# Optimization experiments

Measured on AMD Instinct MI355X. Metric: run time of the kernel, lower is better.

## Reference

```python
import jax, jax.numpy as jnp
import numpy as np

N_TREES = 10
N_DEPTH = 8
IN_DIM = 2048
CLASSES = 1000
BATCH = 16384
N_DECISION = 2 ** N_DEPTH - 1          # 255
N_LEAF = 2 ** (N_DEPTH + 1)            # 512 (module's own convention)


def _tiling_pattern():
    # Static gather pattern mapping each (leaf, depth) slot to an index into
    # the packed [decision_p, 1 - decision_p] tensor, exactly as in the source.
    tp = np.zeros((N_LEAF, N_DEPTH), dtype=np.int32)
    dec_idx = 0
    for n in range(N_DEPTH):
        j = 0
        for _ in range(2 ** n):
            rep = 2 ** (N_DEPTH - n)
            tp[j:j + rep, n] = dec_idx
            j += rep
            tp[j:j + rep, n] = N_DECISION + dec_idx
            j += rep
            dec_idx += 1
    return tp.reshape(-1)

FLAT_PATTERN = jnp.asarray(_tiling_pattern())  # [N_LEAF * N_DEPTH]


def setup_inputs() -> dict:
    key = jax.random.key(0)
    kx, kd, kl = jax.random.split(key, 3)
    x = jax.random.normal(kx, (BATCH, IN_DIM), dtype=jnp.float32)
    # small scale so sigmoid logits are not fully saturated (mimics uniform init)
    w_d = jax.random.normal(kd, (N_TREES, IN_DIM, N_DECISION), dtype=jnp.float32) * 0.02
    w_l = jax.random.normal(kl, (N_TREES, N_LEAF, CLASSES), dtype=jnp.float32)
    return {"x": x, "w_d": w_d, "w_l": w_l}


def reference(x, w_d, w_l):
    # decision probabilities for all trees: [T, B, N_DECISION]
    decision_p = jax.nn.sigmoid(jnp.einsum('bi,tid->tbd', x, w_d))
    # packed [p, 1-p]: [T, B, 2*N_DECISION]
    pack = jnp.concatenate([decision_p, 1.0 - decision_p], axis=-1)
    # static gather -> path probability factors: [T, B, N_LEAF, N_DEPTH]
    mu = pack[..., FLAT_PATTERN].reshape(N_TREES, x.shape[0], N_LEAF, N_DEPTH)
    leaf_prob = jnp.prod(mu, axis=-1)               # [T, B, N_LEAF]
    leaf_p = jax.nn.softmax(w_l, axis=-1)           # [T, N_LEAF, C]
    # sum over trees, then average
    return jnp.einsum('tbl,tlc->bc', leaf_prob, leaf_p) / N_TREES
```

## Files before the change

kernel.cpp:

```cpp
#include <hip/hip_runtime.h>
#include <stdint.h>

#define T_TREES 10
#define IN_DIM  2048
#define BATCH   16384
#define CLASSES 1000
#define NDEC    255
#define NPAD    256
#define K2DIM   (T_TREES * NPAD)
#define NPADC   1024

typedef unsigned short u16;
typedef float floatx4 __attribute__((ext_vector_type(4)));
typedef __bf16 bf16x8 __attribute__((ext_vector_type(8)));

__device__ __forceinline__ u16 f2bf(float f) {
    union { float f; uint32_t u; } v; v.f = f;
    uint32_t u = v.u;
    return (u16)((u + 0x7FFFu + ((u >> 16) & 1u)) >> 16);
}
__device__ __forceinline__ float bf2f(u16 h) {
    union { uint32_t u; float f; } v; v.u = ((uint32_t)h) << 16;
    return v.f;
}

__device__ __forceinline__ void gld16(u16* lds, const u16* g) {
    __builtin_amdgcn_global_load_lds(
        (__attribute__((address_space(1))) const void*)g,
        (__attribute__((address_space(3))) void*)lds,
        16, 0, 0);
}

__global__ __launch_bounds__(256) void cast_x_k(const float4* __restrict__ x,
                                                uint2* __restrict__ xb) {
    int i = blockIdx.x * 256 + threadIdx.x;
    float4 v = x[i];
    uint2 o;
    o.x = (uint32_t)f2bf(v.x) | ((uint32_t)f2bf(v.y) << 16);
    o.y = (uint32_t)f2bf(v.z) | ((uint32_t)f2bf(v.w) << 16);
    xb[i] = o;
}

__global__ void transpose_wd_k(const float* __restrict__ wd, u16* __restrict__ wdT) {
    __shared__ float tile[32][33];
    int tx = threadIdx.x, ty = threadIdx.y;
    int t = blockIdx.z;
    int i0 = blockIdx.x * 32, d0 = blockIdx.y * 32;
#pragma unroll
    for (int r = 0; r < 4; ++r) {
        int i = i0 + ty + r * 8;
        int d = d0 + tx;
        float v = (d < NDEC) ? wd[((size_t)t * IN_DIM + i) * NDEC + d] : 0.0f;
        tile[ty + r * 8][tx] = v;
    }
    __syncthreads();
#pragma unroll
    for (int r = 0; r < 4; ++r) {
        int dd = d0 + ty + r * 8;
        int ii = i0 + tx;
        wdT[((size_t)t * NPAD + dd) * IN_DIM + ii] = f2bf(tile[tx][ty + r * 8]);
    }
}

__global__ __launch_bounds__(256) void softmax_fold_k(const float* __restrict__ wl,
                                                      u16* __restrict__ B2) {
    int wid = threadIdx.x >> 6, lane = threadIdx.x & 63;
    int idx = blockIdx.x * 4 + wid;
    int t = idx >> 8, m = idx & 255;
    const float* r0 = wl + ((size_t)t * 512 + 2 * m) * CLASSES;
    const float* r1 = r0 + CLASSES;
    float v0[16], v1[16];
    float mx0 = -3.0e38f, mx1 = -3.0e38f;
#pragma unroll
    for (int j = 0; j < 16; ++j) {
        int c = lane + 64 * j;
        float a = (c < CLASSES) ? r0[c] : -3.0e38f;
        float b = (c < CLASSES) ? r1[c] : -3.0e38f;
        v0[j] = a; v1[j] = b;
        mx0 = fmaxf(mx0, a); mx1 = fmaxf(mx1, b);
    }
#pragma unroll
    for (int o = 32; o > 0; o >>= 1) {
        mx0 = fmaxf(mx0, __shfl_xor(mx0, o));
        mx1 = fmaxf(mx1, __shfl_xor(mx1, o));
    }
    float s0 = 0.f, s1 = 0.f;
#pragma unroll
    for (int j = 0; j < 16; ++j) {
        int c = lane + 64 * j;
        float e0 = (c < CLASSES) ? __expf(v0[j] - mx0) : 0.f;
        float e1 = (c < CLASSES) ? __expf(v1[j] - mx1) : 0.f;
        v0[j] = e0; v1[j] = e1; s0 += e0; s1 += e1;
    }
#pragma unroll
    for (int o = 32; o > 0; o >>= 1) { s0 += __shfl_xor(s0, o); s1 += __shfl_xor(s1, o); }
    float i0 = 0.1f / s0, i1 = 0.1f / s1;
#pragma unroll
    for (int j = 0; j < 16; ++j) {
        int c = lane + 64 * j;
        float v = (c < CLASSES) ? (v0[j] * i0 + v1[j] * i1) : 0.f;
        B2[(size_t)idx * NPADC + c] = f2bf(v);
    }
}

__global__ void transpose_b2_k(const u16* __restrict__ B2, u16* __restrict__ B2t) {
    __shared__ u16 tile[32][33];
    int tx = threadIdx.x, ty = threadIdx.y;
    int k0 = blockIdx.x * 32, c0 = blockIdx.y * 32;
#pragma unroll
    for (int r = 0; r < 4; ++r)
        tile[ty + r * 8][tx] = B2[(size_t)(k0 + ty + r * 8) * NPADC + c0 + tx];
    __syncthreads();
#pragma unroll
    for (int r = 0; r < 4; ++r)
        B2t[(size_t)(c0 + ty + r * 8) * K2DIM + k0 + tx] = tile[tx][ty + r * 8];
}

template <int EPI, int MINW>
__global__ __launch_bounds__(256, MINW) void gemm_bt(const u16* __restrict__ A,
                                               const u16* __restrict__ B,
                                               void* __restrict__ Cout,
                                               const int K, const long strideBz,
                                               const long strideCz, const int ldc,
                                               const int ncols) {
    __shared__ __align__(16) u16 As[128 * 32];
    __shared__ __align__(16) u16 Bs[128 * 32];
    const int tid  = threadIdx.x;
    const int wid  = tid >> 6;
    const int lane = tid & 63;
    const int wr = wid >> 1, wc = wid & 1;
    const int quad = lane >> 4, t16 = lane & 15;

    const size_t m0 = (size_t)blockIdx.x * 128;
    const size_t n0 = (size_t)blockIdx.y * 128;
    const u16* Ag = A + m0 * (size_t)K;
    const u16* Bg = B + (size_t)blockIdx.z * strideBz + n0 * (size_t)K;

    const int ch0   = wid * 2;
    const int srow0 = ch0 * 16 + (lane >> 2);
    const int skk   = ((lane & 3) ^ ((lane >> 3) & 3)) * 8;
    const u16* ag0 = Ag + (size_t)srow0 * K + skk;
    const u16* ag1 = ag0 + (size_t)16 * K;
    const u16* bg0 = Bg + (size_t)srow0 * K + skk;
    const u16* bg1 = bg0 + (size_t)16 * K;
    u16* lA0 = &As[ch0 * 512];
    u16* lA1 = &As[ch0 * 512 + 512];
    u16* lB0 = &Bs[ch0 * 512];
    u16* lB1 = &Bs[ch0 * 512 + 512];

    const int sw = (quad ^ ((t16 >> 1) & 3)) * 8;

    floatx4 acc[4][4];
#pragma unroll
    for (int i = 0; i < 4; ++i)
#pragma unroll
        for (int j = 0; j < 4; ++j) acc[i][j] = (floatx4){0.f, 0.f, 0.f, 0.f};

    for (int k0 = 0; k0 < K; k0 += 32) {
        gld16(lA0, ag0 + k0);
        gld16(lA1, ag1 + k0);
        gld16(lB0, bg0 + k0);
        gld16(lB1, bg1 + k0);
        __syncthreads();

        bf16x8 af[4], bfr[4];
#pragma unroll
        for (int mi = 0; mi < 4; ++mi)
            af[mi] = *(const bf16x8*)&As[(wr * 64 + mi * 16 + t16) * 32 + sw];
#pragma unroll
        for (int ni = 0; ni < 4; ++ni)
            bfr[ni] = *(const bf16x8*)&Bs[(wc * 64 + ni * 16 + t16) * 32 + sw];
#pragma unroll
        for (int mi = 0; mi < 4; ++mi)
#pragma unroll
            for (int ni = 0; ni < 4; ++ni)
                acc[mi][ni] = __builtin_amdgcn_mfma_f32_16x16x32_bf16(
                    af[mi], bfr[ni], acc[mi][ni], 0, 0, 0);
        __syncthreads();
    }

    if (EPI == 0) {
        u16* C = (u16*)Cout + (size_t)blockIdx.z * strideCz;
#pragma unroll
        for (int mi = 0; mi < 4; ++mi)
#pragma unroll
            for (int r = 0; r < 4; ++r) {
                size_t row = m0 + wr * 64 + mi * 16 + quad * 4 + r;
#pragma unroll
                for (int ni = 0; ni < 4; ++ni) {
                    int col = (int)n0 + wc * 64 + ni * 16 + t16;
                    float v = acc[mi][ni][r];
                    float p = 1.0f / (1.0f + __expf(-v));
                    C[row * (size_t)ldc + col] = f2bf(p);
                }
            }
    } else {
        float* C = (float*)Cout;
#pragma unroll
        for (int mi = 0; mi < 4; ++mi)
#pragma unroll
            for (int r = 0; r < 4; ++r) {
                size_t row = m0 + wr * 64 + mi * 16 + quad * 4 + r;
#pragma unroll
                for (int ni = 0; ni < 4; ++ni) {
                    int col = (int)n0 + wc * 64 + ni * 16 + t16;
                    if (col < ncols) C[row * (size_t)ldc + col] = acc[mi][ni][r];
                }
            }
    }
}

__global__ __launch_bounds__(256) void leafprod_k(const u16* __restrict__ dp,
                                                  u16* __restrict__ lp) {
    __shared__ float P[4][256];
    int wid = threadIdx.x >> 6, lane = threadIdx.x & 63;
    int idx = blockIdx.x * 4 + wid;
    int t = idx >> 14, b = idx & 16383;
    const u16* row = dp + (size_t)idx * NPAD;
#pragma unroll
    for (int j = 0; j < 4; ++j)
        P[wid][lane + 64 * j] = bf2f(row[lane + 64 * j]);
    __syncthreads();
#pragma unroll
    for (int j = 0; j < 4; ++j) {
        int m = lane + 64 * j;
        float prod = 1.0f;
#pragma unroll
        for (int n = 0; n < 8; ++n) {
            int dec  = (1 << n) - 1 + (m >> (8 - n));
            int side = (m >> (7 - n)) & 1;
            float p  = P[wid][dec];
            prod *= side ? (1.0f - p) : p;
        }
        lp[(size_t)b * K2DIM + t * NPAD + m] = f2bf(prod);
    }
}

extern "C" void kernel_launch(void* const* d_in, const int* in_sizes, int n_in,
                              void* d_out, int out_size, void* d_ws, size_t ws_size,
                              hipStream_t stream) {
    const float* x   = (const float*)d_in[0];
    const float* w_d = (const float*)d_in[1];
    const float* w_l = (const float*)d_in[2];
    float* out = (float*)d_out;

    char* w = (char*)d_ws;
    u16* B2t = (u16*)w;
    char* region = w + 5242880;
    u16* xb  = (u16*)region;
    u16* wdT = (u16*)(region + 67108864);
    u16* B2  = (u16*)(region + 67108864 + 10485760);
    u16* lp  = (u16*)region;
    u16* dp  = (u16*)(region + 83886080);

    cast_x_k<<<32768, 256, 0, stream>>>((const float4*)x, (uint2*)xb);
    transpose_wd_k<<<dim3(64, 8, T_TREES), dim3(32, 8), 0, stream>>>(w_d, wdT);
    softmax_fold_k<<<640, 256, 0, stream>>>(w_l, B2);
    transpose_b2_k<<<dim3(80, 32), dim3(32, 8), 0, stream>>>(B2, B2t);
    gemm_bt<0, 3><<<dim3(128, 2, T_TREES), 256, 0, stream>>>(
        xb, wdT, dp, IN_DIM, (long)NPAD * IN_DIM, (long)BATCH * NPAD, NPAD, NPAD);
    leafprod_k<<<40960, 256, 0, stream>>>(dp, lp);
    gemm_bt<1, 4><<<dim3(128, 8, 1), 256, 0, stream>>>(
        lp, B2t, out, K2DIM, 0L, 0L, CLASSES, CLASSES);
}
```

Measured before the change: 583.5 us.

## Fuse leaf-product into first GEMM epilogue and double K-step in second GEMM

The first GEMM now runs each tree's two 128-column halves in a single block. The first half's sigmoid outputs are stashed in LDS, and the second half's epilogue computes the leaf path products directly into lp. This removes the separate leafprod kernel and the dp intermediate write and read. The second GEMM loads two 32-wide K slices per barrier to halve synchronisation count. In exchange, the first GEMM has less grid parallelism (sequential halves) and a large LDS stash that may reduce occupancy.

```diff
diff --git a/kernel.cpp b/kernel.cpp
--- a/kernel.cpp
+++ b/kernel.cpp
@@ -116,15 +116,12 @@
         B2t[(size_t)(c0 + ty + r * 8) * K2DIM + k0 + tx] = tile[tx][ty + r * 8];
 }
 
-template <int EPI, int MINW>
-__global__ __launch_bounds__(256, MINW) void gemm_bt(const u16* __restrict__ A,
-                                               const u16* __restrict__ B,
-                                               void* __restrict__ Cout,
-                                               const int K, const long strideBz,
-                                               const long strideCz, const int ldc,
-                                               const int ncols) {
+__global__ __launch_bounds__(256, 3) void gemm1_fused_k(const u16* __restrict__ A,
+                                                        const u16* __restrict__ Bw,
+                                                        u16* __restrict__ lp) {
     __shared__ __align__(16) u16 As[128 * 32];
     __shared__ __align__(16) u16 Bs[128 * 32];
+    __shared__ u16 stash[128 * 132];
     const int tid  = threadIdx.x;
     const int wid  = tid >> 6;
     const int lane = tid & 63;
@@ -132,108 +129,189 @@
     const int quad = lane >> 4, t16 = lane & 15;
 
     const size_t m0 = (size_t)blockIdx.x * 128;
-    const size_t n0 = (size_t)blockIdx.y * 128;
-    const u16* Ag = A + m0 * (size_t)K;
-    const u16* Bg = B + (size_t)blockIdx.z * strideBz + n0 * (size_t)K;
+    const int t = blockIdx.y;
+    const u16* Ag = A + m0 * (size_t)IN_DIM;
 
     const int ch0   = wid * 2;
     const int srow0 = ch0 * 16 + (lane >> 2);
     const int skk   = ((lane & 3) ^ ((lane >> 3) & 3)) * 8;
-    const u16* ag0 = Ag + (size_t)srow0 * K + skk;
-    const u16* ag1 = ag0 + (size_t)16 * K;
-    const u16* bg0 = Bg + (size_t)srow0 * K + skk;
-    const u16* bg1 = bg0 + (size_t)16 * K;
+    const u16* ag0 = Ag + (size_t)srow0 * IN_DIM + skk;
+    const u16* ag1 = ag0 + (size_t)16 * IN_DIM;
     u16* lA0 = &As[ch0 * 512];
     u16* lA1 = &As[ch0 * 512 + 512];
     u16* lB0 = &Bs[ch0 * 512];
     u16* lB1 = &Bs[ch0 * 512 + 512];
-
     const int sw = (quad ^ ((t16 >> 1) & 3)) * 8;
 
+#pragma unroll 1
+    for (int nh = 0; nh < 2; ++nh) {
+        const u16* Bg  = Bw + ((size_t)t * NPAD + nh * 128) * (size_t)IN_DIM;
+        const u16* bg0 = Bg + (size_t)srow0 * IN_DIM + skk;
+        const u16* bg1 = bg0 + (size_t)16 * IN_DIM;
+
+        floatx4 acc[4][4];
+#pragma unroll
+        for (int i = 0; i < 4; ++i)
+#pragma unroll
+            for (int j = 0; j < 4; ++j) acc[i][j] = (floatx4){0.f, 0.f, 0.f, 0.f};
+
+        for (int k0 = 0; k0 < IN_DIM; k0 += 32) {
+            gld16(lA0, ag0 + k0);
+            gld16(lA1, ag1 + k0);
+            gld16(lB0, bg0 + k0);
+            gld16(lB1, bg1 + k0);
+            __syncthreads();
+
+            bf16x8 af[4], bfr[4];
+#pragma unroll
+            for (int mi = 0; mi < 4; ++mi)
+                af[mi] = *(const bf16x8*)&As[(wr * 64 + mi * 16 + t16) * 32 + sw];
+#pragma unroll
+            for (int ni = 0; ni < 4; ++ni)
+                bfr[ni] = *(const bf16x8*)&Bs[(wc * 64 + ni * 16 + t16) * 32 + sw];
+#pragma unroll
+            for (int mi = 0; mi < 4; ++mi)
+#pragma unroll
+                for (int ni = 0; ni < 4; ++ni)
+                    acc[mi][ni] = __builtin_amdgcn_mfma_f32_16x16x32_bf16(
+                        af[mi], bfr[ni], acc[mi][ni], 0, 0, 0);
+            __syncthreads();
+        }
+
+        if (nh == 0) {
+#pragma unroll
+            for (int mi = 0; mi < 4; ++mi)
+#pragma unroll
+                for (int r = 0; r < 4; ++r) {
+                    int row = wr * 64 + mi * 16 + quad * 4 + r;
+#pragma unroll
+                    for (int ni = 0; ni < 4; ++ni) {
+                        int c = wc * 64 + ni * 16 + t16;
+                        float p = 1.0f / (1.0f + __expf(-acc[mi][ni][r]));
+                        stash[row * 132 + c] = f2bf(p);
+                    }
+                }
+        } else {
+            __syncthreads();
+#pragma unroll
+            for (int mi = 0; mi < 4; ++mi)
+#pragma unroll
+                for (int r = 0; r < 4; ++r) {
+                    int row = wr * 64 + mi * 16 + quad * 4 + r;
+                    size_t grow = m0 + row;
+#pragma unroll
+                    for (int ni = 0; ni < 4; ++ni) {
+                        int c_local = wc * 64 + ni * 16 + t16;
+                        int q = (c_local == 127) ? 0 : (c_local + 1);
+                        float p = 1.0f / (1.0f + __expf(-acc[mi][ni][r]));
+                        if (q == 0) p = bf2f(stash[row * 132 + 127]);
+                        float pre = 1.0f;
+#pragma unroll
+                        for (int n = 0; n < 7; ++n) {
+                            int dec  = (1 << n) - 1 + (q >> (7 - n));
+                            int side = (q >> (6 - n)) & 1;
+                            float f  = bf2f(stash[row * 132 + dec]);
+                            pre *= side ? (1.0f - f) : f;
+                        }
+                        u16 lo = f2bf(pre * p);
+                        u16 hi = f2bf(pre * (1.0f - p));
+                        *(uint32_t*)&lp[grow * K2DIM + (size_t)t * NPAD + 2 * q] =
+                            (uint32_t)lo | ((uint32_t)hi << 16);
+                    }
+                }
+        }
+    }
+}
+
+__global__ __launch_bounds__(256, 4) void gemm2_k(const u16* __restrict__ A,
+                                                  const u16* __restrict__ B,
+                                                  float* __restrict__ C) {
+    __shared__ __align__(16) u16 As0[128 * 32];
+    __shared__ __align__(16) u16 Bs0[128 * 32];
+    __shared__ __align__(16) u16 As1[128 * 32];
+    __shared__ __align__(16) u16 Bs1[128 * 32];
+    const int tid  = threadIdx.x;
+    const int wid  = tid >> 6;
+    const int lane = tid & 63;
+    const int wr = wid >> 1, wc = wid & 1;
+    const int quad = lane >> 4, t16 = lane & 15;
+
+    const size_t m0 = (size_t)blockIdx.x * 128;
+    const size_t n0 = (size_t)blockIdx.y * 128;
+    const u16* Ag = A + m0 * (size_t)K2DIM;
+    const u16* Bg = B + n0 * (size_t)K2DIM;
+
+    const int ch0   = wid * 2;
+    const int srow0 = ch0 * 16 + (lane >> 2);
+    const int skk   = ((lane & 3) ^ ((lane >> 3) & 3)) * 8;
+    const u16* ag0 = Ag + (size_t)srow0 * K2DIM + skk;
+    const u16* ag1 = ag0 + (size_t)16 * K2DIM;
+    const u16* bg0 = Bg + (size_t)srow0 * K2DIM + skk;
+    const u16* bg1 = bg0 + (size_t)16 * K2DIM;
+    const int co = ch0 * 512;
+    const int sw = (quad ^ ((t16 >> 1) & 3)) * 8;
+
     floatx4 acc[4][4];
 #pragma unroll
     for (int i = 0; i < 4; ++i)
 #pragma unroll
         for (int j = 0; j < 4; ++j) acc[i][j] = (floatx4){0.f, 0.f, 0.f, 0.f};
 
-    for (int k0 = 0; k0 < K; k0 += 32) {
-        gld16(lA0, ag0 + k0);
-        gld16(lA1, ag1 + k0);
-        gld16(lB0, bg0 + k0);
-        gld16(lB1, bg1 + k0);
+    for (int k0 = 0; k0 < K2DIM; k0 += 64) {
+        gld16(&As0[co], ag0 + k0);
+        gld16(&As0[co + 512], ag1 + k0);
+        gld16(&Bs0[co], bg0 + k0);
+        gld16(&Bs0[co + 512], bg1 + k0);
+        gld16(&As1[co], ag0 + k0 + 32);
+        gld16(&As1[co + 512], ag1 + k0 + 32);
+        gld16(&Bs1[co], bg0 + k0 + 32);
+        gld16(&Bs1[co + 512], bg1 + k0 + 32);
         __syncthreads();
 
-        bf16x8 af[4], bfr[4];
-#pragma unroll
-        for (int mi = 0; mi < 4; ++mi)
-            af[mi] = *(const bf16x8*)&As[(wr * 64 + mi * 16 + t16) * 32 + sw];
-#pragma unroll
-        for (int ni = 0; ni < 4; ++ni)
-            bfr[ni] = *(const bf16x8*)&Bs[(wc * 64 + ni * 16 + t16) * 32 + sw];
-#pragma unroll
-        for (int mi = 0; mi < 4; ++mi)
+        {
+            bf16x8 af[4], bfr[4];
+#pragma unroll
+            for (int mi = 0; mi < 4; ++mi)
+                af[mi] = *(const bf16x8*)&As0[(wr * 64 + mi * 16 + t16) * 32 + sw];
 #pragma unroll
             for (int ni = 0; ni < 4; ++ni)
-                acc[mi][ni] = __builtin_amdgcn_mfma_f32_16x16x32_bf16(
-                    af[mi], bfr[ni], acc[mi][ni], 0, 0, 0);
+                bfr[ni] = *(const bf16x8*)&Bs0[(wc * 64 + ni * 16 + t16) * 32 + sw];
+#pragma unroll
+            for (int mi = 0; mi < 4; ++mi)
+#pragma unroll
+                for (int ni = 0; ni < 4; ++ni)
+                    acc[mi][ni] = __builtin_amdgcn_mfma_f32_16x16x32_bf16(
+                        af[mi], bfr[ni], acc[mi][ni], 0, 0, 0);
+        }
+        {
+            bf16x8 af[4], bfr[4];
+#pragma unroll
+            for (int mi = 0; mi < 4; ++mi)
+                af[mi] = *(const bf16x8*)&As1[(wr * 64 + mi * 16 + t16) * 32 + sw];
+#pragma unroll
+            for (int ni = 0; ni < 4; ++ni)
+                bfr[ni] = *(const bf16x8*)&Bs1[(wc * 64 + ni * 16 + t16) * 32 + sw];
+#pragma unroll
+            for (int mi = 0; mi < 4; ++mi)
+#pragma unroll
+                for (int ni = 0; ni < 4; ++ni)
+                    acc[mi][ni] = __builtin_amdgcn_mfma_f32_16x16x32_bf16(
+                        af[mi], bfr[ni], acc[mi][ni], 0, 0, 0);
+        }
         __syncthreads();
     }
 
-    if (EPI == 0) {
-        u16* C = (u16*)Cout + (size_t)blockIdx.z * strideCz;
-#pragma unroll
-        for (int mi = 0; mi < 4; ++mi)
-#pragma unroll
-            for (int r = 0; r < 4; ++r) {
-                size_t row = m0 + wr * 64 + mi * 16 + quad * 4 + r;
-#pragma unroll
-                for (int ni = 0; ni < 4; ++ni) {
-                    int col = (int)n0 + wc * 64 + ni * 16 + t16;
-                    float v = acc[mi][ni][r];
-                    float p = 1.0f / (1.0f + __expf(-v));
-                    C[row * (size_t)ldc + col] = f2bf(p);
-                }
+#pragma unroll
+    for (int mi = 0; mi < 4; ++mi)
+#pragma unroll
+        for (int r = 0; r < 4; ++r) {
+            size_t row = m0 + wr * 64 + mi * 16 + quad * 4 + r;
+#pragma unroll
+            for (int ni = 0; ni < 4; ++ni) {
+                int col = (int)n0 + wc * 64 + ni * 16 + t16;
+                if (col < CLASSES) C[row * (size_t)CLASSES + col] = acc[mi][ni][r];
             }
-    } else {
-        float* C = (float*)Cout;
-#pragma unroll
-        for (int mi = 0; mi < 4; ++mi)
-#pragma unroll
-            for (int r = 0; r < 4; ++r) {
-                size_t row = m0 + wr * 64 + mi * 16 + quad * 4 + r;
-#pragma unroll
-                for (int ni = 0; ni < 4; ++ni) {
-                    int col = (int)n0 + wc * 64 + ni * 16 + t16;
-                    if (col < ncols) C[row * (size_t)ldc + col] = acc[mi][ni][r];
-                }
-            }
-    }
-}
-
-__global__ __launch_bounds__(256) void leafprod_k(const u16* __restrict__ dp,
-                                                  u16* __restrict__ lp) {
-    __shared__ float P[4][256];
-    int wid = threadIdx.x >> 6, lane = threadIdx.x & 63;
-    int idx = blockIdx.x * 4 + wid;
-    int t = idx >> 14, b = idx & 16383;
-    const u16* row = dp + (size_t)idx * NPAD;
-#pragma unroll
-    for (int j = 0; j < 4; ++j)
-        P[wid][lane + 64 * j] = bf2f(row[lane + 64 * j]);
-    __syncthreads();
-#pragma unroll
-    for (int j = 0; j < 4; ++j) {
-        int m = lane + 64 * j;
-        float prod = 1.0f;
-#pragma unroll
-        for (int n = 0; n < 8; ++n) {
-            int dec  = (1 << n) - 1 + (m >> (8 - n));
-            int side = (m >> (7 - n)) & 1;
-            float p  = P[wid][dec];
-            prod *= side ? (1.0f - p) : p;
-        }
-        lp[(size_t)b * K2DIM + t * NPAD + m] = f2bf(prod);
-    }
+        }
 }
 
 extern "C" void kernel_launch(void* const* d_in, const int* in_sizes, int n_in,
@@ -250,16 +328,12 @@
     u16* xb  = (u16*)region;
     u16* wdT = (u16*)(region + 67108864);
     u16* B2  = (u16*)(region + 67108864 + 10485760);
-    u16* lp  = (u16*)region;
-    u16* dp  = (u16*)(region + 83886080);
+    u16* lp  = (u16*)(region + 83886080);
 
     cast_x_k<<<32768, 256, 0, stream>>>((const float4*)x, (uint2*)xb);
     transpose_wd_k<<<dim3(64, 8, T_TREES), dim3(32, 8), 0, stream>>>(w_d, wdT);
     softmax_fold_k<<<640, 256, 0, stream>>>(w_l, B2);
     transpose_b2_k<<<dim3(80, 32), dim3(32, 8), 0, stream>>>(B2, B2t);
-    gemm_bt<0, 3><<<dim3(128, 2, T_TREES), 256, 0, stream>>>(
-        xb, wdT, dp, IN_DIM, (long)NPAD * IN_DIM, (long)BATCH * NPAD, NPAD, NPAD);
-    leafprod_k<<<40960, 256, 0, stream>>>(dp, lp);
-    gemm_bt<1, 4><<<dim3(128, 8, 1), 256, 0, stream>>>(
-        lp, B2t, out, K2DIM, 0L, 0L, CLASSES, CLASSES);
-}
+    gemm1_fused_k<<<dim3(128, T_TREES), 256, 0, stream>>>(xb, wdT, lp);
+    gemm2_k<<<dim3(128, 8), 256, 0, stream>>>(lp, B2t, out);
+}
```

Result: slower. 1.110 ms (+90.2%).
